# Kernel tuning notes

Measured on AMD Instinct MI355X. Metric: run time of the kernel, lower is better.

## Reference

```python
import jax, jax.numpy as jnp
import numpy as np
from jax import lax

T, H, I, E = 1024, 1024, 512, 16          # tokens, hidden, moe_intermediate, n_routed_experts
TOP_K, N_GROUP, TOPK_GROUP = 4, 4, 2
N_SHARED = 2
I_SHARED = I * N_SHARED                    # shared-expert intermediate size
ROUTED_SCALE = 2.5


def setup_inputs() -> dict:
    key = jax.random.key(0)
    ks = jax.random.split(key, 9)
    s = lambda k, shape, fan: jax.random.normal(k, shape, jnp.float32) * (fan ** -0.5)
    return {
        "hidden_states": jax.random.normal(ks[0], (T, H), jnp.float32),
        "router_w": s(ks[1], (H, E), H),                 # gate: ReplicatedLinear(H, E)
        "e_bias": jax.random.normal(ks[2], (E,), jnp.float32) * 0.01,  # e_score_correction_bias
        "w_gate": s(ks[3], (E, H, I), H),                # routed experts gate_proj
        "w_up": s(ks[4], (E, H, I), H),                  # routed experts up_proj
        "w_down": s(ks[5], (E, I, H), I),                # routed experts down_proj
        "sw_gate": s(ks[6], (H, I_SHARED), H),           # shared experts gate_proj
        "sw_up": s(ks[7], (H, I_SHARED), H),             # shared experts up_proj
        "sw_down": s(ks[8], (I_SHARED, H), I_SHARED),    # shared experts down_proj
    }


def _grouped_topk_sigmoid(logits, e_bias):
    # DeepSeek-V3 'noaux_tc' grouped top-k with sigmoid scoring.
    scores = jax.nn.sigmoid(logits)                      # [T, E]
    sc = scores + e_bias                                 # biased scores for selection only
    g = sc.reshape(-1, N_GROUP, E // N_GROUP)
    group_scores = lax.top_k(g, 2)[0].sum(-1)            # [T, n_group]: sum of top-2 per group
    _, gidx = lax.top_k(group_scores, TOPK_GROUP)        # [T, topk_group]
    gmask = jax.nn.one_hot(gidx, N_GROUP, dtype=sc.dtype).sum(1)  # [T, n_group]
    emask = jnp.repeat(gmask, E // N_GROUP, axis=1)      # [T, E]
    masked = jnp.where(emask > 0, sc, 0.0)               # sigmoid scores are >=0
    _, tidx = lax.top_k(masked, TOP_K)                   # [T, top_k]
    w = jnp.take_along_axis(scores, tidx, axis=1)        # weights use UNbiased scores
    w = w / (w.sum(-1, keepdims=True) + 1e-20)           # norm_topk_prob=True
    # dense combine weights [T, E]
    combine = (jax.nn.one_hot(tidx, E, dtype=w.dtype) * w[..., None]).sum(1)
    return combine


def reference(hidden_states, router_w, e_bias, w_gate, w_up, w_down,
              sw_gate, sw_up, sw_down):
    x = hidden_states                                    # [T, H]
    logits = x @ router_w                                # [T, E]
    combine = _grouped_topk_sigmoid(logits, e_bias)      # [T, E]

    # routed experts: SiLU-gated MLP per expert, dense-over-experts reference
    gp = jnp.einsum('th,ehi->tei', x, w_gate)            # [T, E, I]
    up = jnp.einsum('th,ehi->tei', x, w_up)
    h = jax.nn.silu(gp) * up
    oe = jnp.einsum('tei,eih->teh', h, w_down)           # [T, E, H]
    routed = jnp.einsum('teh,te->th', oe, combine)       # [T, H]

    # shared experts MLP (reduce_results=False path), fp32 path scales routed only
    shared = (jax.nn.silu(x @ sw_gate) * (x @ sw_up)) @ sw_down  # [T, H]
    return routed * ROUTED_SCALE + shared
```

## Files before the change

### kernel.cpp

```cpp
#include <hip/hip_runtime.h>
#include <stdint.h>

#define T_TOK 1024
#define HDIM  1024
#define IDIM  512
#define NEXP  16
#define ISH   1024
#define MAXT128  48
#define HSLOTS   6144

typedef _Float16 f16;
typedef __attribute__((ext_vector_type(8))) _Float16 f16x8;
typedef __attribute__((ext_vector_type(4))) _Float16 f16x4;
typedef __attribute__((ext_vector_type(4))) float    f32x4;

__device__ __forceinline__ void gld16(const void* g, void* l) {
  __builtin_amdgcn_global_load_lds(
      (__attribute__((address_space(1))) void*)(uintptr_t)g,
      (__attribute__((address_space(3))) void*)(uint32_t)(uintptr_t)l,
      16, 0, 0);
}

__device__ __forceinline__ f16x8 ldsfragA(const f16* buf, int row, int lch) {
  int phys = lch ^ (row & 7);
  return *(const f16x8*)(buf + row * 64 + phys * 8);
}

__device__ __forceinline__ f16x8 ldsfragB(const f16* buf, int n, int kc) {
  int c = kc ^ ((n >> 3) & 7);
  return *(const f16x8*)(buf + n * 72 + c * 8);
}

__device__ __forceinline__ void loadB(const float* __restrict__ W, int ldW,
                                      int kt, int n0, int tid2, float2* v) {
  int p = tid2 & 31, kg = tid2 >> 5;
  const float* src = W + (size_t)(kt + 8 * kg) * ldW + n0 + 2 * p;
#pragma unroll
  for (int r = 0; r < 8; r++) v[r] = *(const float2*)(src + (size_t)r * ldW);
}
__device__ __forceinline__ void writeB(f16* __restrict__ Bs, int nbase, int tid2,
                                       const float2* v) {
  int p = tid2 & 31, kg = tid2 >> 5;
  f16x8 c0, c1;
#pragma unroll
  for (int r = 0; r < 8; r++) { c0[r] = (f16)v[r].x; c1[r] = (f16)v[r].y; }
  int nn = nbase + 2 * p;
  int cc = kg ^ ((nn >> 3) & 7);
  *(f16x8*)(Bs + (size_t)nn * 72 + cc * 8) = c0;
  *(f16x8*)(Bs + (size_t)(nn + 1) * 72 + cc * 8) = c1;
}

__global__ __launch_bounds__(256) void router_kernel(
    const float* __restrict__ x, const float* __restrict__ rw, const float* __restrict__ ebias,
    f16* __restrict__ xh, int* __restrict__ topk_i, float* __restrict__ topk_w) {
  int wave = threadIdx.x >> 6, l = threadIdx.x & 63;
  int t = blockIdx.x * 4 + wave;
  float acc[16];
#pragma unroll
  for (int e = 0; e < 16; e++) acc[e] = 0.f;
#pragma unroll
  for (int i = 0; i < 4; i++) {
    int k = i * 256 + l * 4;
    float4 xv = *(const float4*)(x + (size_t)t * HDIM + k);
    f16x4 h = { (f16)xv.x, (f16)xv.y, (f16)xv.z, (f16)xv.w };
    *(f16x4*)(xh + (size_t)t * HDIM + k) = h;
    const float* xp = &xv.x;
#pragma unroll
    for (int j = 0; j < 4; j++) {
      float xj = xp[j];
      const float4* w4 = (const float4*)(rw + (size_t)(k + j) * 16);
#pragma unroll
      for (int q = 0; q < 4; q++) {
        float4 w = w4[q];
        acc[q*4+0] += xj * w.x; acc[q*4+1] += xj * w.y;
        acc[q*4+2] += xj * w.z; acc[q*4+3] += xj * w.w;
      }
    }
  }
#pragma unroll
  for (int off = 32; off >= 1; off >>= 1)
#pragma unroll
    for (int e = 0; e < 16; e++) acc[e] += __shfl_xor(acc[e], off, 64);

  if (l == 0) {
    float s[16], sc[16];
#pragma unroll
    for (int e = 0; e < 16; e++) {
      s[e] = 1.f / (1.f + __expf(-acc[e]));
      sc[e] = s[e] + ebias[e];
    }
    float gs[4];
#pragma unroll
    for (int g = 0; g < 4; g++) {
      float a = -1e30f, b2 = -1e30f;
#pragma unroll
      for (int j = 0; j < 4; j++) {
        float v = sc[g*4 + j];
        if (v > a) { b2 = a; a = v; } else if (v > b2) { b2 = v; }
      }
      gs[g] = a + b2;
    }
    int g1 = 0;
    for (int g = 1; g < 4; g++) if (gs[g] > gs[g1]) g1 = g;
    int g2 = -1;
    for (int g = 0; g < 4; g++) if (g != g1 && (g2 < 0 || gs[g] > gs[g2])) g2 = g;
    float masked[16];
#pragma unroll
    for (int e = 0; e < 16; e++) {
      int g = e >> 2;
      masked[e] = (g == g1 || g == g2) ? sc[e] : 0.0f;
    }
    int idx[4]; float wv[4]; float denom = 1e-20f;
#pragma unroll
    for (int j = 0; j < 4; j++) {
      int best = 0; float bv = masked[0];
      for (int e = 1; e < 16; e++) if (masked[e] > bv) { bv = masked[e]; best = e; }
      idx[j] = best; wv[j] = s[best]; denom += s[best];
      masked[best] = -1e30f;
    }
#pragma unroll
    for (int j = 0; j < 4; j++) {
      topk_i[t * 4 + j] = idx[j];
      topk_w[t * 4 + j] = wv[j] / denom * 2.5f;
    }
  }
}

__global__ __launch_bounds__(1024) void scatter_kernel(
    const int* __restrict__ tki,
    int* __restrict__ tok, int* __restrict__ slotmap,
    int* __restrict__ tile_e, int* __restrict__ tile_srow,
    int* __restrict__ tile_hb, int* __restrict__ ntl) {
  __shared__ int lcnt[NEXP], lpos[NEXP], lbase[NEXP];
  int t = threadIdx.x;
  if (t < NEXP) { lcnt[t] = 0; lpos[t] = 0; }
  __syncthreads();
  int idx[4];
#pragma unroll
  for (int j = 0; j < 4; j++) idx[j] = tki[t*4+j];
#pragma unroll
  for (int j = 0; j < 4; j++) atomicAdd(&lcnt[idx[j]], 1);
  __syncthreads();
  if (t == 0) {
    int total = 0, slots = 0;
    for (int e = 0; e < NEXP; e++) {
      int c = lcnt[e], nt = (c + 127) >> 7;
      lbase[e] = slots;
      for (int j = 0; j < nt; j++) {
        tile_e[total] = e; tile_srow[total] = j * 128; tile_hb[total] = slots + j * 128; total++;
      }
      slots += nt * 128;
    }
    ntl[0] = total;
  }
  __syncthreads();
#pragma unroll
  for (int j = 0; j < 4; j++) {
    int slot = atomicAdd(&lpos[idx[j]], 1);
    tok[idx[j] * T_TOK + slot] = t;
    slotmap[t * 4 + j] = lbase[idx[j]] + slot;
  }
  __syncthreads();
  int e = t >> 6, s = t & 63;
  int c = lcnt[e];
  int top = ((c + 127) >> 7) << 7;
  for (int s2 = c + s; s2 < top; s2 += 64) tok[e * T_TOK + s2] = 0;
}

__device__ __forceinline__ f32x4 mfma16(f16x8 a, f16x8 b, f32x4 c) {
  return __builtin_amdgcn_mfma_f32_16x16x32_f16(a, b, c, 0, 0, 0);
}

__global__ __launch_bounds__(512, 4) void gu_all(
    const f16* __restrict__ xh,
    const float* __restrict__ sg, const float* __restrict__ su, f16* __restrict__ hsh,
    const float* __restrict__ wg, const float* __restrict__ wu, f16* __restrict__ hbuf,
    const int* __restrict__ tile_e, const int* __restrict__ tile_srow,
    const int* __restrict__ tile_hb, const int* __restrict__ ntl,
    const int* __restrict__ tok) {
  int b = blockIdx.x;
  const float *Bg, *Bu; f16* Hdst;
  int e = 0, srow = 0, mbase, n0, N;
  bool gather = (b >= 128);
  if (!gather) {
    Bg = sg; Bu = su; Hdst = hsh; N = ISH;
    mbase = (b >> 4) * 128; n0 = (b & 15) * 64;
  } else {
    int rb = b - 128, by = rb >> 3;
    if (by >= ntl[0]) return;
    e = tile_e[by]; srow = tile_srow[by]; mbase = tile_hb[by];
    size_t bo = (size_t)e * HDIM * IDIM;
    Bg = wg + bo; Bu = wu + bo; Hdst = hbuf; N = IDIM;
    n0 = (rb & 7) * 64;
  }
  const int K = HDIM;

  __shared__ f16 As[2 * 128 * 64];
  __shared__ f16 Bgs[2 * 64 * 72], Bus[2 * 64 * 72];

  int tid = threadIdx.x, lane = tid & 63, wave = tid >> 6;
  int quad = lane >> 4, l15 = lane & 15;
  int r = lane >> 3, p = lane & 7;

  const f16* gbA[2]; f16* lbA[2];
#pragma unroll
  for (int jj = 0; jj < 2; jj++) {
    int j = wave * 2 + jj;
    int kcol = (p ^ r) << 3;
    int row = j * 8 + r;
    int grow = gather ? tok[e * T_TOK + srow + row] : (mbase + row);
    gbA[jj] = xh + (size_t)grow * K + kcol;
    lbA[jj] = (f16*)As + (j << 9);
  }

  const float* Bmine = (tid < 256) ? Bg : Bu;
  f16* Bsmine = (tid < 256) ? (f16*)Bgs : (f16*)Bus;
  int tid2 = tid & 255;

  int wr = wave >> 1, wc = wave & 1;
  f32x4 zero = {0.f, 0.f, 0.f, 0.f};
  f32x4 aG[2][2], aU[2][2];
#pragma unroll
  for (int mi = 0; mi < 2; mi++)
#pragma unroll
    for (int ni = 0; ni < 2; ni++) { aG[mi][ni] = zero; aU[mi][ni] = zero; }

  float2 v[8];
#pragma unroll
  for (int jj = 0; jj < 2; jj++) gld16(gbA[jj], lbA[jj]);
  loadB(Bmine, N, 0, n0, tid2, v);
  writeB(Bsmine, 0, tid2, v);
  __syncthreads();

  const int nk = K >> 6;
  for (int it = 0; it < nk; ++it) {
    int cb = it & 1, nb = cb ^ 1;
    bool pf = (it + 1 < nk);
    if (pf) {
      int kt = (it + 1) << 6;
#pragma unroll
      for (int jj = 0; jj < 2; jj++) gld16(gbA[jj] + kt, lbA[jj] + nb * 8192);
      loadB(Bmine, N, kt, n0, tid2, v);
    }
    const f16* Ab = (const f16*)As + cb * 8192;
    const f16* Gb = (const f16*)Bgs + cb * 4608;
    const f16* Ub = (const f16*)Bus + cb * 4608;
#pragma unroll
    for (int ks = 0; ks < 2; ks++) {
      int lch = (ks << 2) + quad;
      f16x8 a[2], g[2], u[2];
#pragma unroll
      for (int mi = 0; mi < 2; mi++) a[mi] = ldsfragA(Ab, 32 * wr + 16 * mi + l15, lch);
#pragma unroll
      for (int ni = 0; ni < 2; ni++) {
        g[ni] = ldsfragB(Gb, 32 * wc + 16 * ni + l15, lch);
        u[ni] = ldsfragB(Ub, 32 * wc + 16 * ni + l15, lch);
      }
#pragma unroll
      for (int mi = 0; mi < 2; mi++)
#pragma unroll
        for (int ni = 0; ni < 2; ni++) {
          aG[mi][ni] = mfma16(a[mi], g[ni], aG[mi][ni]);
          aU[mi][ni] = mfma16(a[mi], u[ni], aU[mi][ni]);
        }
    }
    if (pf) writeB(Bsmine + nb * 4608, 0, tid2, v);
    __syncthreads();
  }
#pragma unroll
  for (int mi = 0; mi < 2; mi++)
#pragma unroll
    for (int ni = 0; ni < 2; ni++)
#pragma unroll
      for (int rg = 0; rg < 4; rg++) {
        int m = 32 * wr + 16 * mi + (quad << 2) + rg;
        int n = n0 + 32 * wc + 16 * ni + l15;
        float g = aG[mi][ni][rg], u = aU[mi][ni][rg];
        float val = (g / (1.f + __expf(-g))) * u;
        Hdst[(size_t)(mbase + m) * N + n] = (f16)val;
      }
}

__global__ __launch_bounds__(512, 4) void down_all(
    const f16* __restrict__ hsh, const float* __restrict__ sd,
    const f16* __restrict__ hbuf, const float* __restrict__ wd,
    float* __restrict__ out, f16* __restrict__ odown,
    const int* __restrict__ tile_hb, const int* __restrict__ tile_e,
    const int* __restrict__ ntl) {
  int b = blockIdx.x;
  bool routed = (b >= 64);
  const f16* A; const float* B; int K, abase, n0;
  if (!routed) {
    A = hsh; B = sd; K = ISH;
    abase = (b >> 3) * 128; n0 = (b & 7) * 128;
  } else {
    int rb = b - 64, by = rb >> 3;
    if (by >= ntl[0]) return;
    abase = tile_hb[by];
    A = hbuf; B = wd + (size_t)tile_e[by] * IDIM * HDIM; K = IDIM;
    n0 = (rb & 7) * 128;
  }

  __shared__ f16 As[2 * 128 * 64];
  __shared__ f16 Bs[2 * 128 * 72];

  int tid = threadIdx.x, lane = tid & 63, wave = tid >> 6;
  int quad = lane >> 4, l15 = lane & 15;
  int r = lane >> 3, p = lane & 7;

  const f16* gbA[2]; f16* lbA[2];
#pragma unroll
  for (int jj = 0; jj < 2; jj++) {
    int j = wave * 2 + jj;
    int kcol = (p ^ r) << 3;
    int row = j * 8 + r;
    gbA[jj] = A + (size_t)(abase + row) * K + kcol;
    lbA[jj] = (f16*)As + (j << 9);
  }

  int nb0 = (tid < 256) ? 0 : 64;
  int tid2 = tid & 255;

  int wr = wave >> 1, wc = wave & 1;
  f32x4 zero = {0.f, 0.f, 0.f, 0.f};
  f32x4 ac[2][4];
#pragma unroll
  for (int mi = 0; mi < 2; mi++)
#pragma unroll
    for (int ni = 0; ni < 4; ni++) ac[mi][ni] = zero;

  float2 v[8];
#pragma unroll
  for (int jj = 0; jj < 2; jj++) gld16(gbA[jj], lbA[jj]);
  loadB(B, HDIM, 0, n0 + nb0, tid2, v);
  writeB((f16*)Bs, nb0, tid2, v);
  __syncthreads();

  const int nk = K >> 6;
  for (int it = 0; it < nk; ++it) {
    int cb = it & 1, nb = cb ^ 1;
    bool pf = (it + 1 < nk);
    if (pf) {
      int kt = (it + 1) << 6;
#pragma unroll
      for (int jj = 0; jj < 2; jj++) gld16(gbA[jj] + kt, lbA[jj] + nb * 8192);
      loadB(B, HDIM, kt, n0 + nb0, tid2, v);
    }
    const f16* Ab = (const f16*)As + cb * 8192;
    const f16* Bb = (const f16*)Bs + cb * 9216;
#pragma unroll
    for (int ks = 0; ks < 2; ks++) {
      int lch = (ks << 2) + quad;
      f16x8 a[2], bb[4];
#pragma unroll
      for (int mi = 0; mi < 2; mi++) a[mi] = ldsfragA(Ab, 32 * wr + 16 * mi + l15, lch);
#pragma unroll
      for (int ni = 0; ni < 4; ni++) bb[ni] = ldsfragB(Bb, 64 * wc + 16 * ni + l15, lch);
#pragma unroll
      for (int mi = 0; mi < 2; mi++)
#pragma unroll
        for (int ni = 0; ni < 4; ni++)
          ac[mi][ni] = mfma16(a[mi], bb[ni], ac[mi][ni]);
    }
    if (pf) writeB((f16*)Bs + nb * 9216, nb0, tid2, v);
    __syncthreads();
  }
#pragma unroll
  for (int mi = 0; mi < 2; mi++)
#pragma unroll
    for (int ni = 0; ni < 4; ni++)
#pragma unroll
      for (int rg = 0; rg < 4; rg++) {
        int m = 32 * wr + 16 * mi + (quad << 2) + rg;
        int n = n0 + 64 * wc + 16 * ni + l15;
        if (routed) odown[(size_t)(abase + m) * HDIM + n] = (f16)ac[mi][ni][rg];
        else        out  [(size_t)(abase + m) * HDIM + n] = ac[mi][ni][rg];
      }
}

__global__ __launch_bounds__(256) void combine_kernel(
    const f16* __restrict__ odown, const int* __restrict__ slotmap,
    const float* __restrict__ tkw, float* __restrict__ out) {
  int t = blockIdx.x;
  __shared__ int ss[4]; __shared__ float sw[4];
  if (threadIdx.x < 4) {
    ss[threadIdx.x] = slotmap[t * 4 + threadIdx.x];
    sw[threadIdx.x] = tkw[t * 4 + threadIdx.x];
  }
  __syncthreads();
  int h = threadIdx.x * 4;
  float4 acc = *(const float4*)(out + (size_t)t * HDIM + h);
#pragma unroll
  for (int j = 0; j < 4; j++) {
    f16x4 v = *(const f16x4*)(odown + (size_t)ss[j] * HDIM + h);
    float wj = sw[j];
    acc.x += wj * (float)v[0]; acc.y += wj * (float)v[1];
    acc.z += wj * (float)v[2]; acc.w += wj * (float)v[3];
  }
  *(float4*)(out + (size_t)t * HDIM + h) = acc;
}

extern "C" void kernel_launch(void* const* d_in, const int* in_sizes, int n_in,
                              void* d_out, int out_size, void* d_ws, size_t ws_size,
                              hipStream_t stream) {
  const float* x  = (const float*)d_in[0];
  const float* rw = (const float*)d_in[1];
  const float* eb = (const float*)d_in[2];
  const float* wg = (const float*)d_in[3];
  const float* wu = (const float*)d_in[4];
  const float* wd = (const float*)d_in[5];
  const float* sg = (const float*)d_in[6];
  const float* su = (const float*)d_in[7];
  const float* sd = (const float*)d_in[8];
  float* out = (float*)d_out;
  (void)in_sizes; (void)n_in; (void)out_size; (void)ws_size;

  char* w = (char*)d_ws;
  size_t off = 0;
  auto alloc = [&](size_t b) { void* p = w + off; off = (off + b + 255) & ~(size_t)255; return p; };

  f16* xh   = (f16*)alloc((size_t)T_TOK * HDIM * 2);
  f16* hbuf = (f16*)alloc((size_t)HSLOTS * IDIM * 2);
  f16* hsh  = (f16*)alloc((size_t)T_TOK * ISH * 2);
  f16* odown = (f16*)alloc((size_t)HSLOTS * HDIM * 2);
  int* topk_i = (int*)alloc((size_t)T_TOK * 4 * 4);
  float* topk_w = (float*)alloc((size_t)T_TOK * 4 * 4);
  int* tok  = (int*)alloc((size_t)NEXP * T_TOK * 4);
  int* slotmap = (int*)alloc((size_t)T_TOK * 4 * 4);
  int* tile_e    = (int*)alloc(MAXT128 * 4);
  int* tile_srow = (int*)alloc(MAXT128 * 4);
  int* tile_hb   = (int*)alloc(MAXT128 * 4);
  int* ntl       = (int*)alloc(16);

  router_kernel<<<T_TOK / 4, 256, 0, stream>>>(x, rw, eb, xh, topk_i, topk_w);
  scatter_kernel<<<1, 1024, 0, stream>>>(topk_i, tok, slotmap,
                                         tile_e, tile_srow, tile_hb, ntl);
  gu_all<<<128 + MAXT128 * 8, 512, 0, stream>>>(
      xh, sg, su, hsh, wg, wu, hbuf, tile_e, tile_srow, tile_hb, ntl, tok);
  down_all<<<64 + MAXT128 * 8, 512, 0, stream>>>(
      hsh, sd, hbuf, wd, out, odown, tile_hb, tile_e, ntl);
  combine_kernel<<<T_TOK, 256, 0, stream>>>(odown, slotmap, topk_w, out);
}
```

Measured before the change: 221.5 us.

## Shrink expert and shared GEMM M-tiles from 128 to 64 rows with 256-thread blocks

Halves the M tile in both the gate/up and down GEMMs, moving to 256-thread blocks in which each thread loads both the gate and up B tiles (or both B halves). Expert token padding becomes 64-row granularity, which cuts wasted padded rows and raises the block count for better CU occupancy. In exchange, each B weight tile is reloaded by twice as many blocks, so global weight traffic grows, and per-thread register pressure rises.

```diff
diff --git a/kernel.cpp b/kernel.cpp
--- a/kernel.cpp
+++ b/kernel.cpp
@@ -6,8 +6,8 @@
 #define IDIM  512
 #define NEXP  16
 #define ISH   1024
-#define MAXT128  48
-#define HSLOTS   6144
+#define MAXT64   80
+#define HSLOTS   5120
 
 typedef _Float16 f16;
 typedef __attribute__((ext_vector_type(8))) _Float16 f16x8;
@@ -144,12 +144,12 @@
   if (t == 0) {
     int total = 0, slots = 0;
     for (int e = 0; e < NEXP; e++) {
-      int c = lcnt[e], nt = (c + 127) >> 7;
+      int c = lcnt[e], nt = (c + 63) >> 6;
       lbase[e] = slots;
       for (int j = 0; j < nt; j++) {
-        tile_e[total] = e; tile_srow[total] = j * 128; tile_hb[total] = slots + j * 128; total++;
-      }
-      slots += nt * 128;
+        tile_e[total] = e; tile_srow[total] = j * 64; tile_hb[total] = slots + j * 64; total++;
+      }
+      slots += nt * 64;
     }
     ntl[0] = total;
   }
@@ -163,7 +163,7 @@
   __syncthreads();
   int e = t >> 6, s = t & 63;
   int c = lcnt[e];
-  int top = ((c + 127) >> 7) << 7;
+  int top = ((c + 63) >> 6) << 6;
   for (int s2 = c + s; s2 < top; s2 += 64) tok[e * T_TOK + s2] = 0;
 }
 
@@ -171,7 +171,7 @@
   return __builtin_amdgcn_mfma_f32_16x16x32_f16(a, b, c, 0, 0, 0);
 }
 
-__global__ __launch_bounds__(512, 4) void gu_all(
+__global__ __launch_bounds__(256, 3) void gu_all(
     const f16* __restrict__ xh,
     const float* __restrict__ sg, const float* __restrict__ su, f16* __restrict__ hsh,
     const float* __restrict__ wg, const float* __restrict__ wu, f16* __restrict__ hbuf,
@@ -181,12 +181,12 @@
   int b = blockIdx.x;
   const float *Bg, *Bu; f16* Hdst;
   int e = 0, srow = 0, mbase, n0, N;
-  bool gather = (b >= 128);
+  bool gather = (b >= 256);
   if (!gather) {
     Bg = sg; Bu = su; Hdst = hsh; N = ISH;
-    mbase = (b >> 4) * 128; n0 = (b & 15) * 64;
+    mbase = (b >> 4) * 64; n0 = (b & 15) * 64;
   } else {
-    int rb = b - 128, by = rb >> 3;
+    int rb = b - 256, by = rb >> 3;
     if (by >= ntl[0]) return;
     e = tile_e[by]; srow = tile_srow[by]; mbase = tile_hb[by];
     size_t bo = (size_t)e * HDIM * IDIM;
@@ -195,7 +195,7 @@
   }
   const int K = HDIM;
 
-  __shared__ f16 As[2 * 128 * 64];
+  __shared__ f16 As[2 * 64 * 64];
   __shared__ f16 Bgs[2 * 64 * 72], Bus[2 * 64 * 72];
 
   int tid = threadIdx.x, lane = tid & 63, wave = tid >> 6;
@@ -213,10 +213,6 @@
     lbA[jj] = (f16*)As + (j << 9);
   }
 
-  const float* Bmine = (tid < 256) ? Bg : Bu;
-  f16* Bsmine = (tid < 256) ? (f16*)Bgs : (f16*)Bus;
-  int tid2 = tid & 255;
-
   int wr = wave >> 1, wc = wave & 1;
   f32x4 zero = {0.f, 0.f, 0.f, 0.f};
   f32x4 aG[2][2], aU[2][2];
@@ -225,11 +221,13 @@
 #pragma unroll
     for (int ni = 0; ni < 2; ni++) { aG[mi][ni] = zero; aU[mi][ni] = zero; }
 
-  float2 v[8];
+  float2 vg[8], vu[8];
 #pragma unroll
   for (int jj = 0; jj < 2; jj++) gld16(gbA[jj], lbA[jj]);
-  loadB(Bmine, N, 0, n0, tid2, v);
-  writeB(Bsmine, 0, tid2, v);
+  loadB(Bg, N, 0, n0, tid, vg);
+  loadB(Bu, N, 0, n0, tid, vu);
+  writeB((f16*)Bgs, 0, tid, vg);
+  writeB((f16*)Bus, 0, tid, vu);
   __syncthreads();
 
   const int nk = K >> 6;
@@ -239,10 +237,11 @@
     if (pf) {
       int kt = (it + 1) << 6;
 #pragma unroll
-      for (int jj = 0; jj < 2; jj++) gld16(gbA[jj] + kt, lbA[jj] + nb * 8192);
-      loadB(Bmine, N, kt, n0, tid2, v);
-    }
-    const f16* Ab = (const f16*)As + cb * 8192;
+      for (int jj = 0; jj < 2; jj++) gld16(gbA[jj] + kt, lbA[jj] + nb * 4096);
+      loadB(Bg, N, kt, n0, tid, vg);
+      loadB(Bu, N, kt, n0, tid, vu);
+    }
+    const f16* Ab = (const f16*)As + cb * 4096;
     const f16* Gb = (const f16*)Bgs + cb * 4608;
     const f16* Ub = (const f16*)Bus + cb * 4608;
 #pragma unroll
@@ -264,7 +263,10 @@
           aU[mi][ni] = mfma16(a[mi], u[ni], aU[mi][ni]);
         }
     }
-    if (pf) writeB(Bsmine + nb * 4608, 0, tid2, v);
+    if (pf) {
+      writeB((f16*)Bgs + nb * 4608, 0, tid, vg);
+      writeB((f16*)Bus + nb * 4608, 0, tid, vu);
+    }
     __syncthreads();
   }
 #pragma unroll
@@ -281,27 +283,27 @@
       }
 }
 
-__global__ __launch_bounds__(512, 4) void down_all(
+__global__ __launch_bounds__(256, 3) void down_all(
     const f16* __restrict__ hsh, const float* __restrict__ sd,
     const f16* __restrict__ hbuf, const float* __restrict__ wd,
     float* __restrict__ out, f16* __restrict__ odown,
     const int* __restrict__ tile_hb, const int* __restrict__ tile_e,
     const int* __restrict__ ntl) {
   int b = blockIdx.x;
-  bool routed = (b >= 64);
+  bool routed = (b >= 128);
   const f16* A; const float* B; int K, abase, n0;
   if (!routed) {
     A = hsh; B = sd; K = ISH;
-    abase = (b >> 3) * 128; n0 = (b & 7) * 128;
+    abase = (b >> 3) * 64; n0 = (b & 7) * 128;
   } else {
-    int rb = b - 64, by = rb >> 3;
+    int rb = b - 128, by = rb >> 3;
     if (by >= ntl[0]) return;
     abase = tile_hb[by];
     A = hbuf; B = wd + (size_t)tile_e[by] * IDIM * HDIM; K = IDIM;
     n0 = (rb & 7) * 128;
   }
 
-  __shared__ f16 As[2 * 128 * 64];
+  __shared__ f16 As[2 * 64 * 64];
   __shared__ f16 Bs[2 * 128 * 72];
 
   int tid = threadIdx.x, lane = tid & 63, wave = tid >> 6;
@@ -318,9 +320,6 @@
     lbA[jj] = (f16*)As + (j << 9);
   }
 
-  int nb0 = (tid < 256) ? 0 : 64;
-  int tid2 = tid & 255;
-
   int wr = wave >> 1, wc = wave & 1;
   f32x4 zero = {0.f, 0.f, 0.f, 0.f};
   f32x4 ac[2][4];
@@ -329,11 +328,13 @@
 #pragma unroll
     for (int ni = 0; ni < 4; ni++) ac[mi][ni] = zero;
 
-  float2 v[8];
+  float2 vlo[8], vhi[8];
 #pragma unroll
   for (int jj = 0; jj < 2; jj++) gld16(gbA[jj], lbA[jj]);
-  loadB(B, HDIM, 0, n0 + nb0, tid2, v);
-  writeB((f16*)Bs, nb0, tid2, v);
+  loadB(B, HDIM, 0, n0,      tid, vlo);
+  loadB(B, HDIM, 0, n0 + 64, tid, vhi);
+  writeB((f16*)Bs, 0,  tid, vlo);
+  writeB((f16*)Bs, 64, tid, vhi);
   __syncthreads();
 
   const int nk = K >> 6;
@@ -343,10 +344,11 @@
     if (pf) {
       int kt = (it + 1) << 6;
 #pragma unroll
-      for (int jj = 0; jj < 2; jj++) gld16(gbA[jj] + kt, lbA[jj] + nb * 8192);
-      loadB(B, HDIM, kt, n0 + nb0, tid2, v);
-    }
-    const f16* Ab = (const f16*)As + cb * 8192;
+      for (int jj = 0; jj < 2; jj++) gld16(gbA[jj] + kt, lbA[jj] + nb * 4096);
+      loadB(B, HDIM, kt, n0,      tid, vlo);
+      loadB(B, HDIM, kt, n0 + 64, tid, vhi);
+    }
+    const f16* Ab = (const f16*)As + cb * 4096;
     const f16* Bb = (const f16*)Bs + cb * 9216;
 #pragma unroll
     for (int ks = 0; ks < 2; ks++) {
@@ -362,7 +364,10 @@
         for (int ni = 0; ni < 4; ni++)
           ac[mi][ni] = mfma16(a[mi], bb[ni], ac[mi][ni]);
     }
-    if (pf) writeB((f16*)Bs + nb * 9216, nb0, tid2, v);
+    if (pf) {
+      writeB((f16*)Bs + nb * 9216, 0,  tid, vlo);
+      writeB((f16*)Bs + nb * 9216, 64, tid, vhi);
+    }
     __syncthreads();
   }
 #pragma unroll
@@ -427,17 +432,17 @@
   float* topk_w = (float*)alloc((size_t)T_TOK * 4 * 4);
   int* tok  = (int*)alloc((size_t)NEXP * T_TOK * 4);
   int* slotmap = (int*)alloc((size_t)T_TOK * 4 * 4);
-  int* tile_e    = (int*)alloc(MAXT128 * 4);
-  int* tile_srow = (int*)alloc(MAXT128 * 4);
-  int* tile_hb   = (int*)alloc(MAXT128 * 4);
+  int* tile_e    = (int*)alloc(MAXT64 * 4);
+  int* tile_srow = (int*)alloc(MAXT64 * 4);
+  int* tile_hb   = (int*)alloc(MAXT64 * 4);
   int* ntl       = (int*)alloc(16);
 
   router_kernel<<<T_TOK / 4, 256, 0, stream>>>(x, rw, eb, xh, topk_i, topk_w);
   scatter_kernel<<<1, 1024, 0, stream>>>(topk_i, tok, slotmap,
                                          tile_e, tile_srow, tile_hb, ntl);
-  gu_all<<<128 + MAXT128 * 8, 512, 0, stream>>>(
+  gu_all<<<256 + MAXT64 * 8, 256, 0, stream>>>(
       xh, sg, su, hsh, wg, wu, hbuf, tile_e, tile_srow, tile_hb, ntl, tok);
-  down_all<<<64 + MAXT128 * 8, 512, 0, stream>>>(
+  down_all<<<128 + MAXT64 * 8, 256, 0, stream>>>(
       hsh, sd, hbuf, wd, out, odown, tile_hb, tile_e, ntl);
   combine_kernel<<<T_TOK, 256, 0, stream>>>(odown, slotmap, topk_w, out);
 }
```

Result: slower. 252.4 us (+14.0%).

## Schedule expert tile blocks by XCD so each expert's weights stay in one L2

Applied to the files above, without the earlier changes.

Builds a block schedule in the scatter kernel that assigns every tile of an expert to the same blockIdx modulo 8, which matches round-robin dispatch across the MI355X XCDs. Each expert's gate/up and down weights are then read into a single XCD's L2 rather than being spread across all of them. When an XCD's slots would overflow, tiles fall back to the least-loaded XCD. The shared-expert block mapping is also remapped so the blocks sharing an N slice land on one XCD. This relies on the hardware's dispatch order and adds a small serial scheduling loop in thread 0.

```diff
diff --git a/kernel.cpp b/kernel.cpp
--- a/kernel.cpp
+++ b/kernel.cpp
@@ -8,6 +8,7 @@
 #define ISH   1024
 #define MAXT128  48
 #define HSLOTS   6144
+#define NSCHED   (MAXT128 * 8)
 
 typedef _Float16 f16;
 typedef __attribute__((ext_vector_type(8))) _Float16 f16x8;
@@ -130,10 +131,11 @@
     const int* __restrict__ tki,
     int* __restrict__ tok, int* __restrict__ slotmap,
     int* __restrict__ tile_e, int* __restrict__ tile_srow,
-    int* __restrict__ tile_hb, int* __restrict__ ntl) {
+    int* __restrict__ tile_hb, int* __restrict__ ntl, int* __restrict__ sched) {
   __shared__ int lcnt[NEXP], lpos[NEXP], lbase[NEXP];
   int t = threadIdx.x;
   if (t < NEXP) { lcnt[t] = 0; lpos[t] = 0; }
+  if (t < NSCHED) sched[t] = -1;
   __syncthreads();
   int idx[4];
 #pragma unroll
@@ -143,11 +145,21 @@
   __syncthreads();
   if (t == 0) {
     int total = 0, slots = 0;
+    int sc[8];
+    for (int q = 0; q < 8; q++) sc[q] = 0;
     for (int e = 0; e < NEXP; e++) {
       int c = lcnt[e], nt = (c + 127) >> 7;
       lbase[e] = slots;
       for (int j = 0; j < nt; j++) {
-        tile_e[total] = e; tile_srow[total] = j * 128; tile_hb[total] = slots + j * 128; total++;
+        tile_e[total] = e; tile_srow[total] = j * 128; tile_hb[total] = slots + j * 128;
+        int x = e & 7;
+        if (sc[x] + 8 > MAXT128) {
+          int bx = 0;
+          for (int q = 1; q < 8; q++) if (sc[q] < sc[bx]) bx = q;
+          x = bx;
+        }
+        for (int n = 0; n < 8; n++) { sched[x + 8 * sc[x]] = total * 8 + n; sc[x]++; }
+        total++;
       }
       slots += nt * 128;
     }
@@ -177,21 +189,24 @@
     const float* __restrict__ wg, const float* __restrict__ wu, f16* __restrict__ hbuf,
     const int* __restrict__ tile_e, const int* __restrict__ tile_srow,
     const int* __restrict__ tile_hb, const int* __restrict__ ntl,
-    const int* __restrict__ tok) {
+    const int* __restrict__ tok, const int* __restrict__ sched) {
   int b = blockIdx.x;
   const float *Bg, *Bu; f16* Hdst;
   int e = 0, srow = 0, mbase, n0, N;
   bool gather = (b >= 128);
   if (!gather) {
+    int x = b & 7, s = b >> 3;
     Bg = sg; Bu = su; Hdst = hsh; N = ISH;
-    mbase = (b >> 4) * 128; n0 = (b & 15) * 64;
+    mbase = (s >> 1) * 128;
+    n0 = (x + ((s & 1) << 3)) * 64;
   } else {
-    int rb = b - 128, by = rb >> 3;
-    if (by >= ntl[0]) return;
+    int w = sched[b - 128];
+    if (w < 0) return;
+    int by = w >> 3;
     e = tile_e[by]; srow = tile_srow[by]; mbase = tile_hb[by];
     size_t bo = (size_t)e * HDIM * IDIM;
     Bg = wg + bo; Bu = wu + bo; Hdst = hbuf; N = IDIM;
-    n0 = (rb & 7) * 64;
+    n0 = (w & 7) * 64;
   }
   const int K = HDIM;
 
@@ -286,19 +301,20 @@
     const f16* __restrict__ hbuf, const float* __restrict__ wd,
     float* __restrict__ out, f16* __restrict__ odown,
     const int* __restrict__ tile_hb, const int* __restrict__ tile_e,
-    const int* __restrict__ ntl) {
+    const int* __restrict__ ntl, const int* __restrict__ sched) {
   int b = blockIdx.x;
   bool routed = (b >= 64);
   const f16* A; const float* B; int K, abase, n0;
   if (!routed) {
     A = hsh; B = sd; K = ISH;
-    abase = (b >> 3) * 128; n0 = (b & 7) * 128;
+    n0 = (b & 7) * 128; abase = (b >> 3) * 128;
   } else {
-    int rb = b - 64, by = rb >> 3;
-    if (by >= ntl[0]) return;
+    int w = sched[b - 64];
+    if (w < 0) return;
+    int by = w >> 3;
     abase = tile_hb[by];
     A = hbuf; B = wd + (size_t)tile_e[by] * IDIM * HDIM; K = IDIM;
-    n0 = (rb & 7) * 128;
+    n0 = (w & 7) * 128;
   }
 
   __shared__ f16 As[2 * 128 * 64];
@@ -431,13 +447,14 @@
   int* tile_srow = (int*)alloc(MAXT128 * 4);
   int* tile_hb   = (int*)alloc(MAXT128 * 4);
   int* ntl       = (int*)alloc(16);
+  int* sched     = (int*)alloc(NSCHED * 4);
 
   router_kernel<<<T_TOK / 4, 256, 0, stream>>>(x, rw, eb, xh, topk_i, topk_w);
   scatter_kernel<<<1, 1024, 0, stream>>>(topk_i, tok, slotmap,
-                                         tile_e, tile_srow, tile_hb, ntl);
-  gu_all<<<128 + MAXT128 * 8, 512, 0, stream>>>(
-      xh, sg, su, hsh, wg, wu, hbuf, tile_e, tile_srow, tile_hb, ntl, tok);
-  down_all<<<64 + MAXT128 * 8, 512, 0, stream>>>(
-      hsh, sd, hbuf, wd, out, odown, tile_hb, tile_e, ntl);
+                                         tile_e, tile_srow, tile_hb, ntl, sched);
+  gu_all<<<128 + NSCHED, 512, 0, stream>>>(
+      xh, sg, su, hsh, wg, wu, hbuf, tile_e, tile_srow, tile_hb, ntl, tok, sched);
+  down_all<<<64 + NSCHED, 512, 0, stream>>>(
+      hsh, sd, hbuf, wd, out, odown, tile_hb, tile_e, ntl, sched);
   combine_kernel<<<T_TOK, 256, 0, stream>>>(odown, slotmap, topk_w, out);
 }
```

Measured after the change: 230.5 us. 4.1% more time.
